# Performance work log

Hardware: AMD Instinct MI355X
Metric: run time of the kernel (lower is better)

## Reference

```python
import jax, jax.numpy as jnp
import numpy as np

N_FFT = 128
HOP = 32            # fft_stride
WIN_LEN = 512       # window_length
STRIDE = 128        # MPF stride
FS = 2000.0
BANDS = [(0.0, 100.0), (100.0, 200.0), (200.0, 300.0), (300.0, 500.0), (500.0, 750.0), (750.0, 1000.0)]
FRAME_SIZE = WIN_LEN // HOP   # 16 STFT frames per MPF window
FRAME_STEP = STRIDE // HOP    # 4


def _freq_masks():
    freqs = np.fft.rfftfreq(N_FFT, d=1.0 / FS)  # (F,) Hz
    m = np.stack([(freqs > lo) & (freqs <= hi) for lo, hi in BANDS]).astype(np.float32)  # (K, F)
    return jnp.asarray(m)


def setup_inputs() -> dict:
    key = jax.random.key(0)
    return {"inputs": jax.random.normal(key, (8, 16, 32768), dtype=jnp.float32)}


def reference(inputs) -> jnp.ndarray:
    # inputs: (B, C, T)
    B, C, T = inputs.shape
    window = jnp.hanning(N_FFT).astype(inputs.dtype)  # symmetric hann == torch periodic=False
    wnorm = jnp.linalg.norm(window)

    # --- channelwise STFT (center=False, onesided) ---
    n_frames = 1 + (T - N_FFT) // HOP
    fidx = np.arange(n_frames)[:, None] * HOP + np.arange(N_FFT)[None, :]  # (n_frames, N_FFT)
    frames = inputs[..., fidx] * window                                    # (B, C, n_frames, N_FFT)
    stft = jnp.fft.rfft(frames, axis=-1) / wnorm                           # (B, C, n_frames, F) complex

    # --- unfold STFT frames into MPF windows ---
    n_win = (n_frames - FRAME_SIZE) // FRAME_STEP + 1
    widx = np.arange(n_win)[:, None] * FRAME_STEP + np.arange(FRAME_SIZE)  # (n_win, FRAME_SIZE)
    X = stft[:, :, widx, :]                       # (B, C, n_win, FRAME_SIZE, F)
    X = jnp.transpose(X, (0, 2, 4, 1, 3))         # (B, W, F, C, S)

    # --- cross-spectral density, squared magnitude ---
    csd = jnp.einsum('bwfcs,bwfds->bwfcd', X, X.conj()) / FRAME_SIZE  # (B, W, F, C, C) complex
    P = jnp.abs(csd) ** 2                                             # real (B, W, F, C, C)

    # --- frequency-band averaging ---
    masks = _freq_masks()                                             # (K, F)
    band = jnp.einsum('bwfcd,kf->bwkcd', P, masks) / masks.sum(axis=1)[:, None, None]

    # --- SPD matrix log via eigh ---
    evals, evecs = jnp.linalg.eigh(band)                              # (B,W,K,C), (B,W,K,C,C)
    logv = jnp.nan_to_num(jnp.log(evals), nan=0.0, neginf=0.0)
    out = jnp.einsum('...ie,...e,...je->...ij', evecs, logv, evecs)   # (B, W, K, C, C)

    # time-last layout: (B, K, C, C, W)
    return jnp.transpose(out, (0, 2, 3, 4, 1))
```

## Files before the change

### kernel.cpp

```cpp
#include <hip/hip_runtime.h>
#include <math.h>

#define T_LEN 32768
#define NCH   16
#define NB    8
#define NWIN  252
#define NBAND 6
#define NPAIR 136

typedef float v2f __attribute__((ext_vector_type(2)));

struct PairTab { int c[NPAIR]; int d[NPAIR]; };
constexpr PairTab mkpairs() {
    PairTab P{}; int p = 0;
    for (int c = 0; c < 16; ++c)
        for (int d = c; d < 16; ++d) { P.c[p] = c; P.d[p] = d; ++p; }
    return P;
}
constexpr PairTab PT = mkpairs();

template<int G>
__device__ __forceinline__ void acc_csd(const v2f* __restrict__ X,
                                        v2f* __restrict__ acc)
{
#pragma unroll
    for (int t = 0; t < 17; ++t) {
        const int c = PT.c[G + 8 * t];
        const int d = PT.d[G + 8 * t];
        v2f Xc = X[c], Xd = X[d];
        acc[t] = __builtin_elementwise_fma(Xc, Xd.xx, acc[t]);
        acc[t] = __builtin_elementwise_fma((v2f){Xc.y, -Xc.x}, Xd.yy, acc[t]);
    }
}

#define SWZ(v, imm)  __int_as_float(__builtin_amdgcn_ds_swizzle(__float_as_int(v), (imm)))
#define DPPQ(v, ctl) __int_as_float(__builtin_amdgcn_mov_dpp(__float_as_int(v), (ctl), 0xF, 0xF, true))

__device__ __forceinline__ void bfv(v2f& v, v2f p, v2f tw, v2f twn, v2f sg)
{
    v2f t = __builtin_elementwise_fma(sg, v, p);
    v = __builtin_elementwise_fma(t.xx, tw, t.yy * twn);
}
#define BF2(v, EX, TW, TWN, SG) \
    { v2f p_; p_.x = EX(v.x); p_.y = EX(v.y); bfv(v, p_, TW, TWN, SG); }

__global__ __launch_bounds__(512, 2) void csd_band_kernel(const float* __restrict__ x,
                                                          float* __restrict__ band)
{
    const int w    = blockIdx.x;
    const int b    = blockIdx.y;
    const int tid  = threadIdx.x;
    const int lane = tid & 63;
    const int g    = tid >> 6;
    const int f    = lane + 1;

    __shared__ v2f  X2[2][NCH][64];
    __shared__ v2f  scr[8][2][4][17];
    __shared__ float bl[NBAND][NPAIR];
    __shared__ unsigned char pc_[NPAIR], pd_[NPAIR];

    for (int i = tid; i < NBAND * NPAIR; i += 512) (&bl[0][0])[i] = 0.f;
    if (tid < NPAIR) {
        int rem = tid, c = 0;
        while (rem >= 16 - c) { rem -= 16 - c; ++c; }
        pc_[tid] = (unsigned char)c; pd_[tid] = (unsigned char)(c + rem);
    }

    const double PI = 3.14159265358979323846;
    const float  WI = (float)(1.0 / sqrt(47.625));
    const float wlo = (float)(0.5 - 0.5 * cos(2.0 * PI * (double)lane / 127.0)) * WI;
    const float whi = (float)(0.5 - 0.5 * cos(2.0 * PI * (double)(lane + 64) / 127.0)) * WI;

    const float PIF = 3.14159265358979f;
    float w128r, w128i;
    { float a = -2.f * PIF * (float)lane / 128.f; sincosf(a, &w128i, &w128r); }
    float t32r, t32i, t16r, t16i, t8r, t8i, t4r, t4i, t2r, t2i;
    { float a = (lane & 32) ? -2.f * PIF * (float)(lane & 31) / 64.f : 0.f; sincosf(a, &t32i, &t32r); }
    { float a = (lane & 16) ? -2.f * PIF * (float)(lane & 15) / 32.f : 0.f; sincosf(a, &t16i, &t16r); }
    { float a = (lane &  8) ? -2.f * PIF * (float)(lane &  7) / 16.f : 0.f; sincosf(a, &t8i,  &t8r ); }
    { float a = (lane &  4) ? -2.f * PIF * (float)(lane &  3) /  8.f : 0.f; sincosf(a, &t4i,  &t4r ); }
    { float a = (lane &  2) ? -2.f * PIF * (float)(lane &  1) /  4.f : 0.f; sincosf(a, &t2i,  &t2r ); }
    const v2f TWH  = { w128r,  w128i }, TWHN = { -w128i, w128r };
    const v2f TW32 = { t32r, t32i },    TW32N = { -t32i, t32r };
    const v2f TW16 = { t16r, t16i },    TW16N = { -t16i, t16r };
    const v2f TW8  = { t8r,  t8i  },    TW8N  = { -t8i,  t8r  };
    const v2f TW4  = { t4r,  t4i  },    TW4N  = { -t4i,  t4r  };
    const v2f TW2  = { t2r,  t2i  },    TW2N  = { -t2i,  t2r  };
    const v2f SG32 = { (lane & 32) ? -1.f : 1.f, (lane & 32) ? -1.f : 1.f };
    const v2f SG16 = { (lane & 16) ? -1.f : 1.f, (lane & 16) ? -1.f : 1.f };
    const v2f SG8  = { (lane &  8) ? -1.f : 1.f, (lane &  8) ? -1.f : 1.f };
    const v2f SG4  = { (lane &  4) ? -1.f : 1.f, (lane &  4) ? -1.f : 1.f };
    const v2f SG2  = { (lane &  2) ? -1.f : 1.f, (lane &  2) ? -1.f : 1.f };
    const v2f SG1  = { (lane &  1) ? -1.f : 1.f, (lane &  1) ? -1.f : 1.f };

    const int bp32 = 4 * (lane ^ 32);
    const int La = (int)(__brev((unsigned)(f >> 1)) >> 26);
    const int Lb = (int)(__brev((unsigned)((128 - f) >> 1)) >> 26);
    const int pa = f & 1;

    v2f acc[17];
#pragma unroll
    for (int t = 0; t < 17; ++t) acc[t] = (v2f){0.f, 0.f};

    const float* xp0 = x + (size_t)(b * NCH + g) * T_LEN + (size_t)w * 128;
    const float* xp1 = xp0 + 8 * (size_t)T_LEN;

    __syncthreads();

    for (int s = 0; s < 16; ++s) {
        v2f S0 = (v2f){ xp0[s * 32 + lane],      xp1[s * 32 + lane]      } * wlo;
        v2f S1 = (v2f){ xp0[s * 32 + lane + 64], xp1[s * 32 + lane + 64] } * whi;

        {
            v2f D = S0 - S1;
            S0 = S0 + S1;
            S1 = __builtin_elementwise_fma(D.xx, TWH, D.yy * TWHN);
        }
#define EX32(v) __int_as_float(__builtin_amdgcn_ds_bpermute(bp32, __float_as_int(v)))
#define EX16(v) SWZ(v, 0x401F)
#define EX8(v)  DPPQ(v, 0x128)
#define EX4(v)  SWZ(v, 0x101F)
#define EX2(v)  DPPQ(v, 0x4E)
#define EX1(v)  DPPQ(v, 0xB1)
        BF2(S0, EX32, TW32, TW32N, SG32)
        BF2(S1, EX32, TW32, TW32N, SG32)
        BF2(S0, EX16, TW16, TW16N, SG16)
        BF2(S1, EX16, TW16, TW16N, SG16)
        BF2(S0, EX8,  TW8,  TW8N,  SG8)
        BF2(S1, EX8,  TW8,  TW8N,  SG8)
        BF2(S0, EX4,  TW4,  TW4N,  SG4)
        BF2(S1, EX4,  TW4,  TW4N,  SG4)
        BF2(S0, EX2,  TW2,  TW2N,  SG2)
        BF2(S1, EX2,  TW2,  TW2N,  SG2)
        {
            v2f p_; p_.x = EX1(S0.x); p_.y = EX1(S0.y);
            S0 = __builtin_elementwise_fma(SG1, S0, p_);
        }
        {
            v2f p_; p_.x = EX1(S1.x); p_.y = EX1(S1.y);
            S1 = __builtin_elementwise_fma(SG1, S1, p_);
        }

        scr[g][0][lane >> 4][lane & 15] = S0;
        scr[g][1][lane >> 4][lane & 15] = S1;
        v2f Ua = scr[g][pa][La >> 4][La & 15];
        v2f Ub = scr[g][pa][Lb >> 4][Lb & 15];
        v2f X0 = { 0.5f * (Ua.x + Ub.x), 0.5f * (Ua.y - Ub.y) };
        v2f X1 = { 0.5f * (Ua.y + Ub.y), 0.5f * (Ub.x - Ua.x) };

        const int pp = s & 1;
        X2[pp][g][lane]     = X0;
        X2[pp][g + 8][lane] = X1;
        __syncthreads();

        v2f X[16];
#pragma unroll
        for (int c = 0; c < 16; ++c) X[c] = X2[pp][c][lane];
        switch (g) {
            case 0: acc_csd<0>(X, acc); break;
            case 1: acc_csd<1>(X, acc); break;
            case 2: acc_csd<2>(X, acc); break;
            case 3: acc_csd<3>(X, acc); break;
            case 4: acc_csd<4>(X, acc); break;
            case 5: acc_csd<5>(X, acc); break;
            case 6: acc_csd<6>(X, acc); break;
            default: acc_csd<7>(X, acc); break;
        }
    }

    const int kband = (lane < 6) ? 0 : (lane < 12) ? 1 : (lane < 19) ? 2
                    : (lane < 32) ? 3 : (lane < 48) ? 4 : 5;
#pragma unroll
    for (int t = 0; t < 17; ++t) {
        float vv = fmaf(acc[t].x, acc[t].x, acc[t].y * acc[t].y);
        atomicAdd(&bl[kband][g + 8 * t], vv);
    }
    __syncthreads();

    const float rs[NBAND] = { 1.f/(256.f*6.f), 1.f/(256.f*6.f), 1.f/(256.f*7.f),
                              1.f/(256.f*13.f), 1.f/(256.f*16.f), 1.f/(256.f*16.f) };
    float* bb = band + (size_t)(b * NWIN + w) * (NBAND * 256);
    for (int i = tid; i < NBAND * NPAIR; i += 512) {
        int k = i / NPAIR, p = i - k * NPAIR;
        int c = pc_[p], d = pd_[p];
        float val = bl[k][p] * rs[k];
        bb[k * 256 + c * 16 + d] = val;
        bb[k * 256 + d * 16 + c] = val;
    }
}

__device__ __forceinline__ void tourney(int rr, int j, int& p, int& q)
{
    if (j == 0) { p = 15; q = rr; }
    else { p = (rr + j) % 15; q = (rr + 15 - j) % 15; }
    if (p > q) { int t_ = p; p = q; q = t_; }
}

__global__ __launch_bounds__(512) void eig_log_kernel(const float* __restrict__ band,
                                                      float* __restrict__ out)
{
    const int tid  = threadIdx.x;
    const int g    = tid >> 6;
    const int lane = tid & 63;
    const int m    = blockIdx.x * 8 + g;
    const int k    = m % NBAND;
    const int bw   = m / NBAND;
    const int w    = bw % NWIN;
    const int b    = bw / NWIN;
    const int j    = lane >> 3;
    const int n2   = lane & 7;

    __shared__ float A[8][16][18];
    __shared__ float DT[8][16][18];
    __shared__ float VT[8][16][18];
    __shared__ float lv[8][16];

    const float* M = band + ((size_t)(b * NWIN + w) * NBAND + k) * 256;
#pragma unroll
    for (int it = 0; it < 4; ++it) {
        int i = lane + it * 64, r = i >> 4, c = i & 15;
        A[g][r][c]  = M[i];
        VT[g][r][c] = (r == c) ? 1.f : 0.f;
    }

    for (int sweep = 0; sweep < 4; ++sweep) {
        for (int rr = 0; rr < 15; ++rr) {
            int p, q; tourney(rr, j, p, q);
            float app = A[g][p][p], aqq = A[g][q][q], apq = A[g][p][q];
            float c_ = 1.f, s_ = 0.f;
            if (apq != 0.f) {
                float tau = (aqq - app) / (2.f * apq);
                float t   = copysignf(1.f, tau) / (fabsf(tau) + sqrtf(1.f + tau * tau));
                c_ = 1.f / sqrtf(1.f + t * t);
                s_ = t * c_;
            }
            float2 ap = *(const float2*)&A[g][p][2 * n2];
            float2 aq = *(const float2*)&A[g][q][2 * n2];
            DT[g][2 * n2][p]     = c_ * ap.x - s_ * aq.x;
            DT[g][2 * n2 + 1][p] = c_ * ap.y - s_ * aq.y;
            DT[g][2 * n2][q]     = s_ * ap.x + c_ * aq.x;
            DT[g][2 * n2 + 1][q] = s_ * ap.y + c_ * aq.y;

            float2 dp = *(const float2*)&DT[g][p][2 * n2];
            float2 dq = *(const float2*)&DT[g][q][2 * n2];
            *(float2*)&A[g][p][2 * n2] = make_float2(c_ * dp.x - s_ * dq.x,
                                                     c_ * dp.y - s_ * dq.y);
            *(float2*)&A[g][q][2 * n2] = make_float2(s_ * dp.x + c_ * dq.x,
                                                     s_ * dp.y + c_ * dq.y);
            float2 vp = *(const float2*)&VT[g][p][2 * n2];
            float2 vq = *(const float2*)&VT[g][q][2 * n2];
            *(float2*)&VT[g][p][2 * n2] = make_float2(c_ * vp.x - s_ * vq.x,
                                                      c_ * vp.y - s_ * vq.y);
            *(float2*)&VT[g][q][2 * n2] = make_float2(s_ * vp.x + c_ * vq.x,
                                                      s_ * vp.y + c_ * vq.y);
        }
    }

    if (lane < 16) {
        float l = logf(A[g][lane][lane]);
        if (isnan(l) || isinf(l)) l = 0.f;
        lv[g][lane] = l;
    }

    float* ob = out + (size_t)(b * NBAND + k) * 256 * NWIN;
#pragma unroll
    for (int it = 0; it < 4; ++it) {
        int i = lane + it * 64, c = i >> 4, d = i & 15;
        float sum = 0.f;
#pragma unroll
        for (int e = 0; e < 16; ++e) sum = fmaf(VT[g][e][c] * lv[g][e], VT[g][e][d], sum);
        ob[(size_t)i * NWIN + w] = sum;
    }
}

extern "C" void kernel_launch(void* const* d_in, const int* in_sizes, int n_in,
                              void* d_out, int out_size, void* d_ws, size_t ws_size,
                              hipStream_t stream)
{
    const float* x    = (const float*)d_in[0];
    float*       out  = (float*)d_out;
    float*       band = (float*)d_ws;

    dim3 g1(NWIN, NB), b1(512);
    hipLaunchKernelGGL(csd_band_kernel, g1, b1, 0, stream, x, band);

    dim3 g2(NB * NWIN * NBAND / 8), b2(512);
    hipLaunchKernelGGL(eig_log_kernel, g2, b2, 0, stream, band, out);
}
```

Measured before the change: 355.6 us.

## Compute STFT once into workspace, then accumulate CSD from stored frames

Adds a standalone STFT kernel that computes each frame once and writes it to workspace, plus a new CSD/band kernel that reads the stored frames with 16 waves per block. This removes the fourfold redundant FFT work caused by overlapping MPF windows. In exchange it adds a large intermediate buffer round-trip through global memory and an extra launch. The old fused path remains as a fallback when the workspace is too small.

```diff
diff --git a/kernel.cpp b/kernel.cpp
--- a/kernel.cpp
+++ b/kernel.cpp
@@ -7,6 +7,7 @@
 #define NWIN  252
 #define NBAND 6
 #define NPAIR 136
+#define NFR   1020
 
 typedef float v2f __attribute__((ext_vector_type(2)));
 
@@ -33,6 +34,21 @@
     }
 }
 
+template<int GG>
+__device__ __forceinline__ void acc_csd16(const v2f* __restrict__ X,
+                                          v2f* __restrict__ acc)
+{
+    constexpr int NT = (GG < 8) ? 9 : 8;
+#pragma unroll
+    for (int t = 0; t < NT; ++t) {
+        const int c = PT.c[GG + 16 * t];
+        const int d = PT.d[GG + 16 * t];
+        v2f Xc = X[c], Xd = X[d];
+        acc[t] = __builtin_elementwise_fma(Xc, Xd.xx, acc[t]);
+        acc[t] = __builtin_elementwise_fma((v2f){Xc.y, -Xc.x}, Xd.yy, acc[t]);
+    }
+}
+
 #define SWZ(v, imm)  __int_as_float(__builtin_amdgcn_ds_swizzle(__float_as_int(v), (imm)))
 #define DPPQ(v, ctl) __int_as_float(__builtin_amdgcn_mov_dpp(__float_as_int(v), (ctl), 0xF, 0xF, true))
 
@@ -43,6 +59,180 @@
 }
 #define BF2(v, EX, TW, TWN, SG) \
     { v2f p_; p_.x = EX(v.x); p_.y = EX(v.y); bfv(v, p_, TW, TWN, SG); }
+
+#define EX32(v) __int_as_float(__builtin_amdgcn_ds_bpermute(bp32, __float_as_int(v)))
+#define EX16(v) SWZ(v, 0x401F)
+#define EX8(v)  DPPQ(v, 0x128)
+#define EX4(v)  SWZ(v, 0x101F)
+#define EX2(v)  DPPQ(v, 0x4E)
+#define EX1(v)  DPPQ(v, 0xB1)
+
+#define FFT_LANE_SETUP                                                        \
+    const double PI = 3.14159265358979323846;                                 \
+    const float  WI = (float)(1.0 / sqrt(47.625));                            \
+    const float wlo = (float)(0.5 - 0.5 * cos(2.0 * PI * (double)lane / 127.0)) * WI;        \
+    const float whi = (float)(0.5 - 0.5 * cos(2.0 * PI * (double)(lane + 64) / 127.0)) * WI; \
+    const float PIF = 3.14159265358979f;                                      \
+    float w128r, w128i;                                                       \
+    { float a = -2.f * PIF * (float)lane / 128.f; sincosf(a, &w128i, &w128r); } \
+    float t32r, t32i, t16r, t16i, t8r, t8i, t4r, t4i, t2r, t2i;               \
+    { float a = (lane & 32) ? -2.f * PIF * (float)(lane & 31) / 64.f : 0.f; sincosf(a, &t32i, &t32r); } \
+    { float a = (lane & 16) ? -2.f * PIF * (float)(lane & 15) / 32.f : 0.f; sincosf(a, &t16i, &t16r); } \
+    { float a = (lane &  8) ? -2.f * PIF * (float)(lane &  7) / 16.f : 0.f; sincosf(a, &t8i,  &t8r ); } \
+    { float a = (lane &  4) ? -2.f * PIF * (float)(lane &  3) /  8.f : 0.f; sincosf(a, &t4i,  &t4r ); } \
+    { float a = (lane &  2) ? -2.f * PIF * (float)(lane &  1) /  4.f : 0.f; sincosf(a, &t2i,  &t2r ); } \
+    const v2f TWH  = { w128r,  w128i }, TWHN = { -w128i, w128r };             \
+    const v2f TW32 = { t32r, t32i },    TW32N = { -t32i, t32r };              \
+    const v2f TW16 = { t16r, t16i },    TW16N = { -t16i, t16r };              \
+    const v2f TW8  = { t8r,  t8i  },    TW8N  = { -t8i,  t8r  };              \
+    const v2f TW4  = { t4r,  t4i  },    TW4N  = { -t4i,  t4r  };              \
+    const v2f TW2  = { t2r,  t2i  },    TW2N  = { -t2i,  t2r  };              \
+    const v2f SG32 = { (lane & 32) ? -1.f : 1.f, (lane & 32) ? -1.f : 1.f };  \
+    const v2f SG16 = { (lane & 16) ? -1.f : 1.f, (lane & 16) ? -1.f : 1.f };  \
+    const v2f SG8  = { (lane &  8) ? -1.f : 1.f, (lane &  8) ? -1.f : 1.f };  \
+    const v2f SG4  = { (lane &  4) ? -1.f : 1.f, (lane &  4) ? -1.f : 1.f };  \
+    const v2f SG2  = { (lane &  2) ? -1.f : 1.f, (lane &  2) ? -1.f : 1.f };  \
+    const v2f SG1  = { (lane &  1) ? -1.f : 1.f, (lane &  1) ? -1.f : 1.f };  \
+    const int bp32 = 4 * (lane ^ 32);                                         \
+    const int La = (int)(__brev((unsigned)(f >> 1)) >> 26);                   \
+    const int Lb = (int)(__brev((unsigned)((128 - f) >> 1)) >> 26);           \
+    const int pa = f & 1;
+
+#define FFT_BODY(S0, S1, X0, X1, scrrow)                                      \
+    {                                                                         \
+        v2f D = S0 - S1;                                                      \
+        S0 = S0 + S1;                                                         \
+        S1 = __builtin_elementwise_fma(D.xx, TWH, D.yy * TWHN);               \
+    }                                                                         \
+    BF2(S0, EX32, TW32, TW32N, SG32)                                          \
+    BF2(S1, EX32, TW32, TW32N, SG32)                                          \
+    BF2(S0, EX16, TW16, TW16N, SG16)                                          \
+    BF2(S1, EX16, TW16, TW16N, SG16)                                          \
+    BF2(S0, EX8,  TW8,  TW8N,  SG8)                                           \
+    BF2(S1, EX8,  TW8,  TW8N,  SG8)                                           \
+    BF2(S0, EX4,  TW4,  TW4N,  SG4)                                           \
+    BF2(S1, EX4,  TW4,  TW4N,  SG4)                                           \
+    BF2(S0, EX2,  TW2,  TW2N,  SG2)                                           \
+    BF2(S1, EX2,  TW2,  TW2N,  SG2)                                           \
+    {                                                                         \
+        v2f p_; p_.x = EX1(S0.x); p_.y = EX1(S0.y);                           \
+        S0 = __builtin_elementwise_fma(SG1, S0, p_);                          \
+    }                                                                         \
+    {                                                                         \
+        v2f p_; p_.x = EX1(S1.x); p_.y = EX1(S1.y);                           \
+        S1 = __builtin_elementwise_fma(SG1, S1, p_);                          \
+    }                                                                         \
+    scrrow[0][lane >> 4][lane & 15] = S0;                                     \
+    scrrow[1][lane >> 4][lane & 15] = S1;                                     \
+    v2f Ua = scrrow[pa][La >> 4][La & 15];                                    \
+    v2f Ub = scrrow[pa][Lb >> 4][Lb & 15];                                    \
+    v2f X0 = { 0.5f * (Ua.x + Ub.x), 0.5f * (Ua.y - Ub.y) };                  \
+    v2f X1 = { 0.5f * (Ua.y + Ub.y), 0.5f * (Ub.x - Ua.x) };
+
+__global__ __launch_bounds__(512) void stft_kernel(const float* __restrict__ x,
+                                                   v2f* __restrict__ stft)
+{
+    const int tid  = threadIdx.x;
+    const int lane = tid & 63;
+    const int g    = tid >> 6;
+    const int task = blockIdx.x * 8 + g;
+    const int fr   = task % NFR;
+    const int pb   = task / NFR;
+    const int pair = pb & 7, b = pb >> 3;
+    const int f    = lane + 1;
+
+    __shared__ v2f scr[8][2][4][17];
+
+    FFT_LANE_SETUP
+
+    const float* xp0 = x + (size_t)(b * NCH + pair) * T_LEN + (size_t)fr * 32;
+    const float* xp1 = xp0 + 8 * (size_t)T_LEN;
+
+    v2f S0 = (v2f){ xp0[lane],      xp1[lane]      } * wlo;
+    v2f S1 = (v2f){ xp0[lane + 64], xp1[lane + 64] } * whi;
+
+    FFT_BODY(S0, S1, X0, X1, scr[g])
+
+    stft[((size_t)(b * NCH + pair)     * NFR + fr) * 64 + lane] = X0;
+    stft[((size_t)(b * NCH + pair + 8) * NFR + fr) * 64 + lane] = X1;
+}
+
+__global__ __launch_bounds__(1024) void csd_band_kernel2(const v2f* __restrict__ stft,
+                                                         float* __restrict__ band)
+{
+    const int w    = blockIdx.x;
+    const int b    = blockIdx.y;
+    const int tid  = threadIdx.x;
+    const int lane = tid & 63;
+    const int gg   = tid >> 6;
+
+    __shared__ float bl[NBAND][NPAIR];
+    __shared__ unsigned char pc_[NPAIR], pd_[NPAIR];
+
+    for (int i = tid; i < NBAND * NPAIR; i += 1024) (&bl[0][0])[i] = 0.f;
+    if (tid < NPAIR) {
+        int rem = tid, c = 0;
+        while (rem >= 16 - c) { rem -= 16 - c; ++c; }
+        pc_[tid] = (unsigned char)c; pd_[tid] = (unsigned char)(c + rem);
+    }
+
+    v2f acc[9];
+#pragma unroll
+    for (int t = 0; t < 9; ++t) acc[t] = (v2f){0.f, 0.f};
+
+    const v2f* base = stft + ((size_t)(b * NCH) * NFR + (size_t)(4 * w)) * 64 + lane;
+
+    __syncthreads();
+
+#pragma unroll 1
+    for (int j = 0; j < 16; ++j) {
+        v2f X[16];
+#pragma unroll
+        for (int c = 0; c < 16; ++c)
+            X[c] = base[(size_t)c * (NFR * 64) + j * 64];
+        switch (gg) {
+            case 0:  acc_csd16<0>(X, acc);  break;
+            case 1:  acc_csd16<1>(X, acc);  break;
+            case 2:  acc_csd16<2>(X, acc);  break;
+            case 3:  acc_csd16<3>(X, acc);  break;
+            case 4:  acc_csd16<4>(X, acc);  break;
+            case 5:  acc_csd16<5>(X, acc);  break;
+            case 6:  acc_csd16<6>(X, acc);  break;
+            case 7:  acc_csd16<7>(X, acc);  break;
+            case 8:  acc_csd16<8>(X, acc);  break;
+            case 9:  acc_csd16<9>(X, acc);  break;
+            case 10: acc_csd16<10>(X, acc); break;
+            case 11: acc_csd16<11>(X, acc); break;
+            case 12: acc_csd16<12>(X, acc); break;
+            case 13: acc_csd16<13>(X, acc); break;
+            case 14: acc_csd16<14>(X, acc); break;
+            default: acc_csd16<15>(X, acc); break;
+        }
+    }
+
+    const int kband = (lane < 6) ? 0 : (lane < 12) ? 1 : (lane < 19) ? 2
+                    : (lane < 32) ? 3 : (lane < 48) ? 4 : 5;
+#pragma unroll
+    for (int t = 0; t < 9; ++t) {
+        int p = gg + 16 * t;
+        if (p < NPAIR) {
+            float vv = fmaf(acc[t].x, acc[t].x, acc[t].y * acc[t].y);
+            atomicAdd(&bl[kband][p], vv);
+        }
+    }
+    __syncthreads();
+
+    const float rs[NBAND] = { 1.f/(256.f*6.f), 1.f/(256.f*6.f), 1.f/(256.f*7.f),
+                              1.f/(256.f*13.f), 1.f/(256.f*16.f), 1.f/(256.f*16.f) };
+    float* bb = band + (size_t)(b * NWIN + w) * (NBAND * 256);
+    for (int i = tid; i < NBAND * NPAIR; i += 1024) {
+        int k = i / NPAIR, p = i - k * NPAIR;
+        int c = pc_[p], d = pd_[p];
+        float val = bl[k][p] * rs[k];
+        bb[k * 256 + c * 16 + d] = val;
+        bb[k * 256 + d * 16 + c] = val;
+    }
+}
 
 __global__ __launch_bounds__(512, 2) void csd_band_kernel(const float* __restrict__ x,
                                                           float* __restrict__ band)
@@ -66,37 +256,7 @@
         pc_[tid] = (unsigned char)c; pd_[tid] = (unsigned char)(c + rem);
     }
 
-    const double PI = 3.14159265358979323846;
-    const float  WI = (float)(1.0 / sqrt(47.625));
-    const float wlo = (float)(0.5 - 0.5 * cos(2.0 * PI * (double)lane / 127.0)) * WI;
-    const float whi = (float)(0.5 - 0.5 * cos(2.0 * PI * (double)(lane + 64) / 127.0)) * WI;
-
-    const float PIF = 3.14159265358979f;
-    float w128r, w128i;
-    { float a = -2.f * PIF * (float)lane / 128.f; sincosf(a, &w128i, &w128r); }
-    float t32r, t32i, t16r, t16i, t8r, t8i, t4r, t4i, t2r, t2i;
-    { float a = (lane & 32) ? -2.f * PIF * (float)(lane & 31) / 64.f : 0.f; sincosf(a, &t32i, &t32r); }
-    { float a = (lane & 16) ? -2.f * PIF * (float)(lane & 15) / 32.f : 0.f; sincosf(a, &t16i, &t16r); }
-    { float a = (lane &  8) ? -2.f * PIF * (float)(lane &  7) / 16.f : 0.f; sincosf(a, &t8i,  &t8r ); }
-    { float a = (lane &  4) ? -2.f * PIF * (float)(lane &  3) /  8.f : 0.f; sincosf(a, &t4i,  &t4r ); }
-    { float a = (lane &  2) ? -2.f * PIF * (float)(lane &  1) /  4.f : 0.f; sincosf(a, &t2i,  &t2r ); }
-    const v2f TWH  = { w128r,  w128i }, TWHN = { -w128i, w128r };
-    const v2f TW32 = { t32r, t32i },    TW32N = { -t32i, t32r };
-    const v2f TW16 = { t16r, t16i },    TW16N = { -t16i, t16r };
-    const v2f TW8  = { t8r,  t8i  },    TW8N  = { -t8i,  t8r  };
-    const v2f TW4  = { t4r,  t4i  },    TW4N  = { -t4i,  t4r  };
-    const v2f TW2  = { t2r,  t2i  },    TW2N  = { -t2i,  t2r  };
-    const v2f SG32 = { (lane & 32) ? -1.f : 1.f, (lane & 32) ? -1.f : 1.f };
-    const v2f SG16 = { (lane & 16) ? -1.f : 1.f, (lane & 16) ? -1.f : 1.f };
-    const v2f SG8  = { (lane &  8) ? -1.f : 1.f, (lane &  8) ? -1.f : 1.f };
-    const v2f SG4  = { (lane &  4) ? -1.f : 1.f, (lane &  4) ? -1.f : 1.f };
-    const v2f SG2  = { (lane &  2) ? -1.f : 1.f, (lane &  2) ? -1.f : 1.f };
-    const v2f SG1  = { (lane &  1) ? -1.f : 1.f, (lane &  1) ? -1.f : 1.f };
-
-    const int bp32 = 4 * (lane ^ 32);
-    const int La = (int)(__brev((unsigned)(f >> 1)) >> 26);
-    const int Lb = (int)(__brev((unsigned)((128 - f) >> 1)) >> 26);
-    const int pa = f & 1;
+    FFT_LANE_SETUP
 
     v2f acc[17];
 #pragma unroll
@@ -111,42 +271,7 @@
         v2f S0 = (v2f){ xp0[s * 32 + lane],      xp1[s * 32 + lane]      } * wlo;
         v2f S1 = (v2f){ xp0[s * 32 + lane + 64], xp1[s * 32 + lane + 64] } * whi;
 
-        {
-            v2f D = S0 - S1;
-            S0 = S0 + S1;
-            S1 = __builtin_elementwise_fma(D.xx, TWH, D.yy * TWHN);
-        }
-#define EX32(v) __int_as_float(__builtin_amdgcn_ds_bpermute(bp32, __float_as_int(v)))
-#define EX16(v) SWZ(v, 0x401F)
-#define EX8(v)  DPPQ(v, 0x128)
-#define EX4(v)  SWZ(v, 0x101F)
-#define EX2(v)  DPPQ(v, 0x4E)
-#define EX1(v)  DPPQ(v, 0xB1)
-        BF2(S0, EX32, TW32, TW32N, SG32)
-        BF2(S1, EX32, TW32, TW32N, SG32)
-        BF2(S0, EX16, TW16, TW16N, SG16)
-        BF2(S1, EX16, TW16, TW16N, SG16)
-        BF2(S0, EX8,  TW8,  TW8N,  SG8)
-        BF2(S1, EX8,  TW8,  TW8N,  SG8)
-        BF2(S0, EX4,  TW4,  TW4N,  SG4)
-        BF2(S1, EX4,  TW4,  TW4N,  SG4)
-        BF2(S0, EX2,  TW2,  TW2N,  SG2)
-        BF2(S1, EX2,  TW2,  TW2N,  SG2)
-        {
-            v2f p_; p_.x = EX1(S0.x); p_.y = EX1(S0.y);
-            S0 = __builtin_elementwise_fma(SG1, S0, p_);
-        }
-        {
-            v2f p_; p_.x = EX1(S1.x); p_.y = EX1(S1.y);
-            S1 = __builtin_elementwise_fma(SG1, S1, p_);
-        }
-
-        scr[g][0][lane >> 4][lane & 15] = S0;
-        scr[g][1][lane >> 4][lane & 15] = S1;
-        v2f Ua = scr[g][pa][La >> 4][La & 15];
-        v2f Ub = scr[g][pa][Lb >> 4][Lb & 15];
-        v2f X0 = { 0.5f * (Ua.x + Ub.x), 0.5f * (Ua.y - Ub.y) };
-        v2f X1 = { 0.5f * (Ua.y + Ub.y), 0.5f * (Ub.x - Ua.x) };
+        FFT_BODY(S0, S1, X0, X1, scr[g])
 
         const int pp = s & 1;
         X2[pp][g][lane]     = X0;
@@ -281,8 +406,19 @@
     float*       out  = (float*)d_out;
     float*       band = (float*)d_ws;
 
-    dim3 g1(NWIN, NB), b1(512);
-    hipLaunchKernelGGL(csd_band_kernel, g1, b1, 0, stream, x, band);
+    const size_t BAND_BYTES = (size_t)NB * NWIN * NBAND * 256 * 4;
+    const size_t STFT_BYTES = (size_t)NB * NCH * NFR * 64 * 8;
+
+    if (ws_size >= BAND_BYTES + STFT_BYTES) {
+        v2f* stft = (v2f*)((char*)d_ws + BAND_BYTES);
+        hipLaunchKernelGGL(stft_kernel, dim3(NB * 8 * NFR / 8), dim3(512), 0, stream,
+                           x, stft);
+        hipLaunchKernelGGL(csd_band_kernel2, dim3(NWIN, NB), dim3(1024), 0, stream,
+                           stft, band);
+    } else {
+        hipLaunchKernelGGL(csd_band_kernel, dim3(NWIN, NB), dim3(512), 0, stream,
+                           x, band);
+    }
 
     dim3 g2(NB * NWIN * NBAND / 8), b2(512);
     hipLaunchKernelGGL(eig_log_kernel, g2, b2, 0, stream, band, out);
```

New measurement: 468.1 us. 1.32x slower.

## Fuse CSD band kernel with Jacobi eigen-log kernel via shared-memory aliasing

Applied to the files above, without the earlier changes.

Merges the two kernels into one: after band accumulation, six of the eight waves each run the Jacobi eigensolver and matrix log on one band matrix, reading directly from shared memory instead of a global workspace. Shared buffers for the FFT stage are aliased with the eigen-stage buffers to keep LDS usage down. This removes the global round-trip of band matrices and one launch, but it leaves two waves idle during the eigen phase and cuts eigen parallelism to 2016 blocks of six active waves.

```diff
diff --git a/kernel.cpp b/kernel.cpp
--- a/kernel.cpp
+++ b/kernel.cpp
@@ -44,8 +44,22 @@
 #define BF2(v, EX, TW, TWN, SG) \
     { v2f p_; p_.x = EX(v.x); p_.y = EX(v.y); bfv(v, p_, TW, TWN, SG); }
 
-__global__ __launch_bounds__(512, 2) void csd_band_kernel(const float* __restrict__ x,
-                                                          float* __restrict__ band)
+#define EX32(v) __int_as_float(__builtin_amdgcn_ds_bpermute(bp32, __float_as_int(v)))
+#define EX16(v) SWZ(v, 0x401F)
+#define EX8(v)  DPPQ(v, 0x128)
+#define EX4(v)  SWZ(v, 0x101F)
+#define EX2(v)  DPPQ(v, 0x4E)
+#define EX1(v)  DPPQ(v, 0xB1)
+
+__device__ __forceinline__ void tourney(int rr, int j, int& p, int& q)
+{
+    if (j == 0) { p = 15; q = rr; }
+    else { p = (rr + j) % 15; q = (rr + 15 - j) % 15; }
+    if (p > q) { int t_ = p; p = q; q = t_; }
+}
+
+__global__ __launch_bounds__(512, 2) void csd_eig_kernel(const float* __restrict__ x,
+                                                         float* __restrict__ out)
 {
     const int w    = blockIdx.x;
     const int b    = blockIdx.y;
@@ -54,17 +68,17 @@
     const int g    = tid >> 6;
     const int f    = lane + 1;
 
-    __shared__ v2f  X2[2][NCH][64];
-    __shared__ v2f  scr[8][2][4][17];
+    __shared__ __align__(16) char shraw[25088];
+    v2f  (*X2)[NCH][64]  = (v2f (*)[NCH][64])shraw;
+    v2f  (*scr)[2][4][17] = (v2f (*)[2][4][17])(shraw + 16384);
+    float (*A_)[16][18]  = (float (*)[16][18])shraw;
+    float (*DT_)[16][18] = (float (*)[16][18])(shraw + 6912);
+    float (*VT_)[16][18] = (float (*)[16][18])(shraw + 13824);
+    float (*lv_)[16]     = (float (*)[16])(shraw + 20736);
+
     __shared__ float bl[NBAND][NPAIR];
-    __shared__ unsigned char pc_[NPAIR], pd_[NPAIR];
 
     for (int i = tid; i < NBAND * NPAIR; i += 512) (&bl[0][0])[i] = 0.f;
-    if (tid < NPAIR) {
-        int rem = tid, c = 0;
-        while (rem >= 16 - c) { rem -= 16 - c; ++c; }
-        pc_[tid] = (unsigned char)c; pd_[tid] = (unsigned char)(c + rem);
-    }
 
     const double PI = 3.14159265358979323846;
     const float  WI = (float)(1.0 / sqrt(47.625));
@@ -116,12 +130,6 @@
             S0 = S0 + S1;
             S1 = __builtin_elementwise_fma(D.xx, TWH, D.yy * TWHN);
         }
-#define EX32(v) __int_as_float(__builtin_amdgcn_ds_bpermute(bp32, __float_as_int(v)))
-#define EX16(v) SWZ(v, 0x401F)
-#define EX8(v)  DPPQ(v, 0x128)
-#define EX4(v)  SWZ(v, 0x101F)
-#define EX2(v)  DPPQ(v, 0x4E)
-#define EX1(v)  DPPQ(v, 0xB1)
         BF2(S0, EX32, TW32, TW32N, SG32)
         BF2(S1, EX32, TW32, TW32N, SG32)
         BF2(S0, EX16, TW16, TW16N, SG16)
@@ -177,99 +185,69 @@
     }
     __syncthreads();
 
-    const float rs[NBAND] = { 1.f/(256.f*6.f), 1.f/(256.f*6.f), 1.f/(256.f*7.f),
-                              1.f/(256.f*13.f), 1.f/(256.f*16.f), 1.f/(256.f*16.f) };
-    float* bb = band + (size_t)(b * NWIN + w) * (NBAND * 256);
-    for (int i = tid; i < NBAND * NPAIR; i += 512) {
-        int k = i / NPAIR, p = i - k * NPAIR;
-        int c = pc_[p], d = pd_[p];
-        float val = bl[k][p] * rs[k];
-        bb[k * 256 + c * 16 + d] = val;
-        bb[k * 256 + d * 16 + c] = val;
-    }
-}
-
-__device__ __forceinline__ void tourney(int rr, int j, int& p, int& q)
-{
-    if (j == 0) { p = 15; q = rr; }
-    else { p = (rr + j) % 15; q = (rr + 15 - j) % 15; }
-    if (p > q) { int t_ = p; p = q; q = t_; }
-}
-
-__global__ __launch_bounds__(512) void eig_log_kernel(const float* __restrict__ band,
-                                                      float* __restrict__ out)
-{
-    const int tid  = threadIdx.x;
-    const int g    = tid >> 6;
-    const int lane = tid & 63;
-    const int m    = blockIdx.x * 8 + g;
-    const int k    = m % NBAND;
-    const int bw   = m / NBAND;
-    const int w    = bw % NWIN;
-    const int b    = bw / NWIN;
-    const int j    = lane >> 3;
-    const int n2   = lane & 7;
-
-    __shared__ float A[8][16][18];
-    __shared__ float DT[8][16][18];
-    __shared__ float VT[8][16][18];
-    __shared__ float lv[8][16];
-
-    const float* M = band + ((size_t)(b * NWIN + w) * NBAND + k) * 256;
-#pragma unroll
-    for (int it = 0; it < 4; ++it) {
-        int i = lane + it * 64, r = i >> 4, c = i & 15;
-        A[g][r][c]  = M[i];
-        VT[g][r][c] = (r == c) ? 1.f : 0.f;
-    }
-
-    for (int sweep = 0; sweep < 4; ++sweep) {
-        for (int rr = 0; rr < 15; ++rr) {
-            int p, q; tourney(rr, j, p, q);
-            float app = A[g][p][p], aqq = A[g][q][q], apq = A[g][p][q];
-            float c_ = 1.f, s_ = 0.f;
-            if (apq != 0.f) {
-                float tau = (aqq - app) / (2.f * apq);
-                float t   = copysignf(1.f, tau) / (fabsf(tau) + sqrtf(1.f + tau * tau));
-                c_ = 1.f / sqrtf(1.f + t * t);
-                s_ = t * c_;
+    if (g < 6) {
+        const int jp = lane >> 3;
+        const int n2 = lane & 7;
+
+        const float cnt = (g <= 1) ? 6.f : (g == 2) ? 7.f : (g == 3) ? 13.f : 16.f;
+        const float rsg = 1.f / (256.f * cnt);
+#pragma unroll
+        for (int it = 0; it < 4; ++it) {
+            int i = lane + it * 64, r = i >> 4, c = i & 15;
+            int mn = r < c ? r : c, mx = r < c ? c : r;
+            int p = (mn * (33 - mn)) / 2 + (mx - mn);
+            A_[g][r][c]  = bl[g][p] * rsg;
+            VT_[g][r][c] = (r == c) ? 1.f : 0.f;
+        }
+
+        for (int sweep = 0; sweep < 4; ++sweep) {
+            for (int rr = 0; rr < 15; ++rr) {
+                int p, q; tourney(rr, jp, p, q);
+                float app = A_[g][p][p], aqq = A_[g][q][q], apq = A_[g][p][q];
+                float c_ = 1.f, s_ = 0.f;
+                if (apq != 0.f) {
+                    float tau = (aqq - app) / (2.f * apq);
+                    float t   = copysignf(1.f, tau) / (fabsf(tau) + sqrtf(1.f + tau * tau));
+                    c_ = 1.f / sqrtf(1.f + t * t);
+                    s_ = t * c_;
+                }
+                float2 ap = *(const float2*)&A_[g][p][2 * n2];
+                float2 aq = *(const float2*)&A_[g][q][2 * n2];
+                DT_[g][2 * n2][p]     = c_ * ap.x - s_ * aq.x;
+                DT_[g][2 * n2 + 1][p] = c_ * ap.y - s_ * aq.y;
+                DT_[g][2 * n2][q]     = s_ * ap.x + c_ * aq.x;
+                DT_[g][2 * n2 + 1][q] = s_ * ap.y + c_ * aq.y;
+
+                float2 dp = *(const float2*)&DT_[g][p][2 * n2];
+                float2 dq = *(const float2*)&DT_[g][q][2 * n2];
+                *(float2*)&A_[g][p][2 * n2] = make_float2(c_ * dp.x - s_ * dq.x,
+                                                          c_ * dp.y - s_ * dq.y);
+                *(float2*)&A_[g][q][2 * n2] = make_float2(s_ * dp.x + c_ * dq.x,
+                                                          s_ * dp.y + c_ * dq.y);
+                float2 vp = *(const float2*)&VT_[g][p][2 * n2];
+                float2 vq = *(const float2*)&VT_[g][q][2 * n2];
+                *(float2*)&VT_[g][p][2 * n2] = make_float2(c_ * vp.x - s_ * vq.x,
+                                                           c_ * vp.y - s_ * vq.y);
+                *(float2*)&VT_[g][q][2 * n2] = make_float2(s_ * vp.x + c_ * vq.x,
+                                                           s_ * vp.y + c_ * vq.y);
             }
-            float2 ap = *(const float2*)&A[g][p][2 * n2];
-            float2 aq = *(const float2*)&A[g][q][2 * n2];
-            DT[g][2 * n2][p]     = c_ * ap.x - s_ * aq.x;
-            DT[g][2 * n2 + 1][p] = c_ * ap.y - s_ * aq.y;
-            DT[g][2 * n2][q]     = s_ * ap.x + c_ * aq.x;
-            DT[g][2 * n2 + 1][q] = s_ * ap.y + c_ * aq.y;
-
-            float2 dp = *(const float2*)&DT[g][p][2 * n2];
-            float2 dq = *(const float2*)&DT[g][q][2 * n2];
-            *(float2*)&A[g][p][2 * n2] = make_float2(c_ * dp.x - s_ * dq.x,
-                                                     c_ * dp.y - s_ * dq.y);
-            *(float2*)&A[g][q][2 * n2] = make_float2(s_ * dp.x + c_ * dq.x,
-                                                     s_ * dp.y + c_ * dq.y);
-            float2 vp = *(const float2*)&VT[g][p][2 * n2];
-            float2 vq = *(const float2*)&VT[g][q][2 * n2];
-            *(float2*)&VT[g][p][2 * n2] = make_float2(c_ * vp.x - s_ * vq.x,
-                                                      c_ * vp.y - s_ * vq.y);
-            *(float2*)&VT[g][q][2 * n2] = make_float2(s_ * vp.x + c_ * vq.x,
-                                                      s_ * vp.y + c_ * vq.y);
-        }
-    }
-
-    if (lane < 16) {
-        float l = logf(A[g][lane][lane]);
-        if (isnan(l) || isinf(l)) l = 0.f;
-        lv[g][lane] = l;
-    }
-
-    float* ob = out + (size_t)(b * NBAND + k) * 256 * NWIN;
-#pragma unroll
-    for (int it = 0; it < 4; ++it) {
-        int i = lane + it * 64, c = i >> 4, d = i & 15;
-        float sum = 0.f;
-#pragma unroll
-        for (int e = 0; e < 16; ++e) sum = fmaf(VT[g][e][c] * lv[g][e], VT[g][e][d], sum);
-        ob[(size_t)i * NWIN + w] = sum;
+        }
+
+        if (lane < 16) {
+            float l = logf(A_[g][lane][lane]);
+            if (isnan(l) || isinf(l)) l = 0.f;
+            lv_[g][lane] = l;
+        }
+
+        float* ob = out + (size_t)(b * NBAND + g) * 256 * NWIN;
+#pragma unroll
+        for (int it = 0; it < 4; ++it) {
+            int i = lane + it * 64, c = i >> 4, d = i & 15;
+            float sum = 0.f;
+#pragma unroll
+            for (int e = 0; e < 16; ++e) sum = fmaf(VT_[g][e][c] * lv_[g][e], VT_[g][e][d], sum);
+            ob[(size_t)i * NWIN + w] = sum;
+        }
     }
 }
 
@@ -277,13 +255,10 @@
                               void* d_out, int out_size, void* d_ws, size_t ws_size,
                               hipStream_t stream)
 {
-    const float* x    = (const float*)d_in[0];
-    float*       out  = (float*)d_out;
-    float*       band = (float*)d_ws;
+    const float* x   = (const float*)d_in[0];
+    float*       out = (float*)d_out;
+    (void)d_ws; (void)ws_size;
 
     dim3 g1(NWIN, NB), b1(512);
-    hipLaunchKernelGGL(csd_band_kernel, g1, b1, 0, stream, x, band);
-
-    dim3 g2(NB * NWIN * NBAND / 8), b2(512);
-    hipLaunchKernelGGL(eig_log_kernel, g2, b2, 0, stream, band, out);
-}
+    hipLaunchKernelGGL(csd_eig_kernel, g1, b1, 0, stream, x, out);
+}
```

Result: slower. 423.7 us (+19.1%).

## Run two Jacobi eigensolves per wavefront with float4 LDS rows

Applied to the files above, without the earlier changes.

The Jacobi eigen kernel now gives each matrix a 32-thread half-wavefront instead of a full wavefront. Each thread updates four columns with float4 LDS accesses, so one block handles 16 matrices and the grid is halved. The CSD kernel's Hann window setup switches from double-precision to single-precision cos. The aim is more matrices per wavefront and fewer LDS instructions per rotation, at the cost of more LDS per block and four scalar transposed stores per row, which may cause bank conflicts.

```diff
diff --git a/kernel.cpp b/kernel.cpp
--- a/kernel.cpp
+++ b/kernel.cpp
@@ -9,6 +9,7 @@
 #define NPAIR 136
 
 typedef float v2f __attribute__((ext_vector_type(2)));
+typedef float v4f __attribute__((ext_vector_type(4)));
 
 struct PairTab { int c[NPAIR]; int d[NPAIR]; };
 constexpr PairTab mkpairs() {
@@ -66,12 +67,11 @@
         pc_[tid] = (unsigned char)c; pd_[tid] = (unsigned char)(c + rem);
     }
 
-    const double PI = 3.14159265358979323846;
-    const float  WI = (float)(1.0 / sqrt(47.625));
-    const float wlo = (float)(0.5 - 0.5 * cos(2.0 * PI * (double)lane / 127.0)) * WI;
-    const float whi = (float)(0.5 - 0.5 * cos(2.0 * PI * (double)(lane + 64) / 127.0)) * WI;
-
     const float PIF = 3.14159265358979f;
+    const float WI  = 1.f / sqrtf(47.625f);
+    const float wlo = (0.5f - 0.5f * cosf(2.f * PIF * (float)lane / 127.f)) * WI;
+    const float whi = (0.5f - 0.5f * cosf(2.f * PIF * (float)(lane + 64) / 127.f)) * WI;
+
     float w128r, w128i;
     { float a = -2.f * PIF * (float)lane / 128.f; sincosf(a, &w128i, &w128r); }
     float t32r, t32i, t16r, t16i, t8r, t8i, t4r, t4i, t2r, t2i;
@@ -200,33 +200,39 @@
                                                       float* __restrict__ out)
 {
     const int tid  = threadIdx.x;
-    const int g    = tid >> 6;
-    const int lane = tid & 63;
-    const int m    = blockIdx.x * 8 + g;
+    const int half = tid >> 5;
+    const int sub  = tid & 31;
+    const int m    = blockIdx.x * 16 + half;
     const int k    = m % NBAND;
     const int bw   = m / NBAND;
     const int w    = bw % NWIN;
     const int b    = bw / NWIN;
-    const int j    = lane >> 3;
-    const int n2   = lane & 7;
-
-    __shared__ float A[8][16][18];
-    __shared__ float DT[8][16][18];
-    __shared__ float VT[8][16][18];
-    __shared__ float lv[8][16];
-
-    const float* M = band + ((size_t)(b * NWIN + w) * NBAND + k) * 256;
-#pragma unroll
-    for (int it = 0; it < 4; ++it) {
-        int i = lane + it * 64, r = i >> 4, c = i & 15;
-        A[g][r][c]  = M[i];
-        VT[g][r][c] = (r == c) ? 1.f : 0.f;
+    const int jp   = sub >> 2;
+    const int n4   = sub & 3;
+
+    __shared__ v4f A4[16][16][5];
+    __shared__ v4f D4[16][16][5];
+    __shared__ v4f V4[16][16][5];
+    __shared__ float lv[16][16];
+
+    float* Af = (float*)&A4[half][0][0];
+    float* Df = (float*)&D4[half][0][0];
+    float* Vf = (float*)&V4[half][0][0];
+
+    const v4f* M4 = (const v4f*)(band + ((size_t)(b * NWIN + w) * NBAND + k) * 256);
+#pragma unroll
+    for (int it = 0; it < 2; ++it) {
+        int t = sub + it * 32;
+        int r = t >> 2, n = t & 3;
+        A4[half][r][n] = M4[t];
+        V4[half][r][n] = (v4f){ (float)(r == 4 * n),     (float)(r == 4 * n + 1),
+                                (float)(r == 4 * n + 2), (float)(r == 4 * n + 3) };
     }
 
     for (int sweep = 0; sweep < 4; ++sweep) {
         for (int rr = 0; rr < 15; ++rr) {
-            int p, q; tourney(rr, j, p, q);
-            float app = A[g][p][p], aqq = A[g][q][q], apq = A[g][p][q];
+            int p, q; tourney(rr, jp, p, q);
+            float app = Af[p * 20 + p], aqq = Af[q * 20 + q], apq = Af[p * 20 + q];
             float c_ = 1.f, s_ = 0.f;
             if (apq != 0.f) {
                 float tau = (aqq - app) / (2.f * apq);
@@ -234,41 +240,41 @@
                 c_ = 1.f / sqrtf(1.f + t * t);
                 s_ = t * c_;
             }
-            float2 ap = *(const float2*)&A[g][p][2 * n2];
-            float2 aq = *(const float2*)&A[g][q][2 * n2];
-            DT[g][2 * n2][p]     = c_ * ap.x - s_ * aq.x;
-            DT[g][2 * n2 + 1][p] = c_ * ap.y - s_ * aq.y;
-            DT[g][2 * n2][q]     = s_ * ap.x + c_ * aq.x;
-            DT[g][2 * n2 + 1][q] = s_ * ap.y + c_ * aq.y;
-
-            float2 dp = *(const float2*)&DT[g][p][2 * n2];
-            float2 dq = *(const float2*)&DT[g][q][2 * n2];
-            *(float2*)&A[g][p][2 * n2] = make_float2(c_ * dp.x - s_ * dq.x,
-                                                     c_ * dp.y - s_ * dq.y);
-            *(float2*)&A[g][q][2 * n2] = make_float2(s_ * dp.x + c_ * dq.x,
-                                                     s_ * dp.y + c_ * dq.y);
-            float2 vp = *(const float2*)&VT[g][p][2 * n2];
-            float2 vq = *(const float2*)&VT[g][q][2 * n2];
-            *(float2*)&VT[g][p][2 * n2] = make_float2(c_ * vp.x - s_ * vq.x,
-                                                      c_ * vp.y - s_ * vq.y);
-            *(float2*)&VT[g][q][2 * n2] = make_float2(s_ * vp.x + c_ * vq.x,
-                                                      s_ * vp.y + c_ * vq.y);
-        }
-    }
-
-    if (lane < 16) {
-        float l = logf(A[g][lane][lane]);
+            v4f Ap = A4[half][p][n4], Aq = A4[half][q][n4];
+            v4f Wp = c_ * Ap - s_ * Aq;
+            v4f Wq = s_ * Ap + c_ * Aq;
+            Df[(4 * n4 + 0) * 20 + p] = Wp.x;
+            Df[(4 * n4 + 1) * 20 + p] = Wp.y;
+            Df[(4 * n4 + 2) * 20 + p] = Wp.z;
+            Df[(4 * n4 + 3) * 20 + p] = Wp.w;
+            Df[(4 * n4 + 0) * 20 + q] = Wq.x;
+            Df[(4 * n4 + 1) * 20 + q] = Wq.y;
+            Df[(4 * n4 + 2) * 20 + q] = Wq.z;
+            Df[(4 * n4 + 3) * 20 + q] = Wq.w;
+
+            v4f Dp = D4[half][p][n4], Dq = D4[half][q][n4];
+            A4[half][p][n4] = c_ * Dp - s_ * Dq;
+            A4[half][q][n4] = s_ * Dp + c_ * Dq;
+            v4f Vp = V4[half][p][n4], Vq = V4[half][q][n4];
+            V4[half][p][n4] = c_ * Vp - s_ * Vq;
+            V4[half][q][n4] = s_ * Vp + c_ * Vq;
+        }
+    }
+
+    if (sub < 16) {
+        float l = logf(Af[sub * 20 + sub]);
         if (isnan(l) || isinf(l)) l = 0.f;
-        lv[g][lane] = l;
+        lv[half][sub] = l;
     }
 
     float* ob = out + (size_t)(b * NBAND + k) * 256 * NWIN;
 #pragma unroll
-    for (int it = 0; it < 4; ++it) {
-        int i = lane + it * 64, c = i >> 4, d = i & 15;
+    for (int it = 0; it < 8; ++it) {
+        int i = sub + it * 32, c = i >> 4, d = i & 15;
         float sum = 0.f;
 #pragma unroll
-        for (int e = 0; e < 16; ++e) sum = fmaf(VT[g][e][c] * lv[g][e], VT[g][e][d], sum);
+        for (int e = 0; e < 16; ++e)
+            sum = fmaf(Vf[e * 20 + c] * lv[half][e], Vf[e * 20 + d], sum);
         ob[(size_t)i * NWIN + w] = sum;
     }
 }
@@ -284,6 +290,6 @@
     dim3 g1(NWIN, NB), b1(512);
     hipLaunchKernelGGL(csd_band_kernel, g1, b1, 0, stream, x, band);
 
-    dim3 g2(NB * NWIN * NBAND / 8), b2(512);
+    dim3 g2(NB * NWIN * NBAND / 16), b2(512);
     hipLaunchKernelGGL(eig_log_kernel, g2, b2, 0, stream, band, out);
 }
```

After: 354.1 us. Within noise of the previous version (-0.4%).
